# Kernel optimization log

Measured on AMD Instinct MI355X. Metric: run time of the kernel, lower is better.

## Reference

```python
import jax, jax.numpy as jnp
import numpy as np
from math import factorial

D = 2          # qudit dimension
L = 13         # number of qudits: state dim = D**L = 8192
J, K = 0, 1    # levels coupled by the gate
CUTOFF = 10    # Taylor truncation order
INDEX = set(range(13))


def _series(z, parity):
    # sum_{i=1..CUTOFF, i%2==parity} z**i / i!   (truncated exp split into even/odd parts)
    s = jnp.zeros((), dtype=jnp.complex64)
    for i in range(1, CUTOFF + 1):
        if i % 2 == parity:
            s = s + z ** i / factorial(i)
    return s


def _gate(theta):
    # single-qudit RX gate matrix, truncated-Taylor version matching the torch code
    z = (-0.5j) * theta.astype(jnp.complex64)
    odd = _series(z, 1)   # ~ -i sin(theta/2)
    even = _series(z, 0)  # ~ cos(theta/2) - 1
    M = jnp.eye(D, dtype=jnp.complex64)
    M = M.at[J, K].add(odd)
    M = M.at[K, J].add(odd)
    M = M.at[J, J].add(even)
    M = M.at[K, K].add(even)
    return M


def setup_inputs() -> dict:
    key = jax.random.key(0)
    k1, k2, k3 = jax.random.split(key, 3)
    dim = D ** L
    return {
        "x_real": jax.random.normal(k1, (dim, 64), dtype=jnp.float32),
        "x_imag": jax.random.normal(k2, (dim, 64), dtype=jnp.float32),
        "angle": jax.random.normal(k3, (L,), dtype=jnp.float32),
    }


def reference(x_real, x_imag, angle):
    x = x_real.astype(jnp.complex64) + 1j * x_imag.astype(jnp.complex64)
    eye = jnp.eye(D, dtype=jnp.complex64)
    U = jnp.eye(1, dtype=jnp.complex64)
    for i in range(L):  # fixed structural loop over qudits (13 iterations)
        M = _gate(angle[i]) if i in INDEX else eye
        U = jnp.kron(U, M)
    out = U @ x  # [D^L, B] complex64
    return jnp.stack([out.real, out.imag])  # [2, D^L, B] float32
```

## Files before the change

kernel.cpp:

```cpp
#include <hip/hip_runtime.h>

#define PLANE (8192 * 64)

typedef float f4 __attribute__((ext_vector_type(4)));
typedef float f2 __attribute__((ext_vector_type(2)));

__device__ __forceinline__ void gate_coeffs(float theta, float& a, float& s) {
    float t = 0.5f * theta;
    float u = t * t;
    s = t * (1.f + u * (-1.f/6.f + u * (1.f/120.f + u * (-1.f/5040.f + u * (1.f/362880.f)))));
    a = 1.f + u * (-0.5f + u * (1.f/24.f + u * (-1.f/720.f + u * (1.f/40320.f + u * (-1.f/3628800.f)))));
}

__device__ __forceinline__ void bf(f4& v0, f4& v1, float a, float s) {
    f4 n0, n1;
    n0.x = a * v0.x + s * v1.y;  n0.y = a * v0.y - s * v1.x;
    n0.z = a * v0.z + s * v1.w;  n0.w = a * v0.w - s * v1.z;
    n1.x = a * v1.x + s * v0.y;  n1.y = a * v1.y - s * v0.x;
    n1.z = a * v1.z + s * v0.w;  n1.w = a * v1.w - s * v0.z;
    v0 = n0; v1 = n1;
}

__global__ __launch_bounds__(256) void rx_low(const float* __restrict__ xr,
                                              const float* __restrict__ xi,
                                              const float* __restrict__ angle,
                                              f4* __restrict__ ws4) {
    __shared__ f4 l4[64 * 16];
    const int t = threadIdx.x, bid = blockIdx.x;
    const int g = bid >> 1, half = bid & 1;
    const int cp = t & 15, rq = t >> 4;

    const f2* xr2 = (const f2*)xr;
    const f2* xi2 = (const f2*)xi;

    {
        float a0, s0, a1, s1;
        gate_coeffs(angle[12], a0, s0);
        gate_coeffs(angle[11], a1, s1);
        f4 v[4];
        #pragma unroll
        for (int k = 0; k < 4; ++k) {
            int gi = (g * 64 + 4 * rq + k) * 32 + half * 16 + cp;
            f2 re = __builtin_nontemporal_load(xr2 + gi);
            f2 im = __builtin_nontemporal_load(xi2 + gi);
            v[k] = (f4){re.x, im.x, re.y, im.y};
        }
        bf(v[0], v[1], a0, s0); bf(v[2], v[3], a0, s0);
        bf(v[0], v[2], a1, s1); bf(v[1], v[3], a1, s1);
        #pragma unroll
        for (int k = 0; k < 4; ++k) l4[(4 * rq + k) * 16 + cp] = v[k];
    }
    __syncthreads();

    {
        float a2, s2, a3, s3;
        gate_coeffs(angle[10], a2, s2);
        gate_coeffs(angle[9],  a3, s3);
        int base = ((rq >> 2) << 4) | (rq & 3);
        f4 w0 = l4[(base     ) * 16 + cp], w1 = l4[(base +  4) * 16 + cp];
        f4 w2 = l4[(base +  8) * 16 + cp], w3 = l4[(base + 12) * 16 + cp];
        bf(w0, w1, a2, s2); bf(w2, w3, a2, s2);
        bf(w0, w2, a3, s3); bf(w1, w3, a3, s3);
        l4[(base     ) * 16 + cp] = w0; l4[(base +  4) * 16 + cp] = w1;
        l4[(base +  8) * 16 + cp] = w2; l4[(base + 12) * 16 + cp] = w3;
    }
    __syncthreads();

    {
        float a4, s4, a5, s5;
        gate_coeffs(angle[8], a4, s4);
        gate_coeffs(angle[7], a5, s5);
        f4 w0 = l4[(rq     ) * 16 + cp], w1 = l4[(rq + 16) * 16 + cp];
        f4 w2 = l4[(rq + 32) * 16 + cp], w3 = l4[(rq + 48) * 16 + cp];
        bf(w0, w1, a4, s4); bf(w2, w3, a4, s4);
        bf(w0, w2, a5, s5); bf(w1, w3, a5, s5);
        const int cp32 = half * 16 + cp, q = cp32 >> 3, cb = cp32 & 7;
        const int e = g * 8 + cb;
        ws4[(size_t)((rq     ) * 4 + q) * 1024 + e] = w0;
        ws4[(size_t)((rq + 16) * 4 + q) * 1024 + e] = w1;
        ws4[(size_t)((rq + 32) * 4 + q) * 1024 + e] = w2;
        ws4[(size_t)((rq + 48) * 4 + q) * 1024 + e] = w3;
    }
}

__global__ __launch_bounds__(256) void rx_high(const float* __restrict__ angle,
                                               const f4* __restrict__ ws4,
                                               float* __restrict__ out) {
    __shared__ f4 l4[128 * 8];
    const int t = threadIdx.x, bid = blockIdx.x;
    const int m = bid >> 2, q = bid & 3;
    const int cp = t & 7, hq = t >> 3;

    {
        float a5, s5, a6, s6;
        gate_coeffs(angle[1], a5, s5);
        gate_coeffs(angle[0], a6, s6);
        const f4* src = ws4 + (size_t)(m * 4 + q) * 1024;
        f4 v0 = src[(hq     ) * 8 + cp], v1 = src[(hq + 32) * 8 + cp];
        f4 v2 = src[(hq + 64) * 8 + cp], v3 = src[(hq + 96) * 8 + cp];
        bf(v0, v1, a5, s5); bf(v2, v3, a5, s5);
        bf(v0, v2, a6, s6); bf(v1, v3, a6, s6);
        l4[(hq     ) * 8 + cp] = v0; l4[(hq + 32) * 8 + cp] = v1;
        l4[(hq + 64) * 8 + cp] = v2; l4[(hq + 96) * 8 + cp] = v3;
    }
    __syncthreads();

    {
        float a3, s3, a4, s4;
        gate_coeffs(angle[3], a3, s3);
        gate_coeffs(angle[2], a4, s4);
        int base = ((hq >> 3) << 5) | (hq & 7);
        f4 w0 = l4[(base     ) * 8 + cp], w1 = l4[(base +  8) * 8 + cp];
        f4 w2 = l4[(base + 16) * 8 + cp], w3 = l4[(base + 24) * 8 + cp];
        bf(w0, w1, a3, s3); bf(w2, w3, a3, s3);
        bf(w0, w2, a4, s4); bf(w1, w3, a4, s4);
        l4[(base     ) * 8 + cp] = w0; l4[(base +  8) * 8 + cp] = w1;
        l4[(base + 16) * 8 + cp] = w2; l4[(base + 24) * 8 + cp] = w3;
    }
    __syncthreads();

    {
        float a1, s1, a2, s2;
        gate_coeffs(angle[5], a1, s1);
        gate_coeffs(angle[4], a2, s2);
        int b = ((hq >> 1) << 3) | (hq & 1);
        f4 w0 = l4[(b    ) * 8 + cp], w1 = l4[(b + 2) * 8 + cp];
        f4 w2 = l4[(b + 4) * 8 + cp], w3 = l4[(b + 6) * 8 + cp];
        bf(w0, w1, a1, s1); bf(w2, w3, a1, s1);
        bf(w0, w2, a2, s2); bf(w1, w3, a2, s2);
        l4[(b    ) * 8 + cp] = w0; l4[(b + 2) * 8 + cp] = w1;
        l4[(b + 4) * 8 + cp] = w2; l4[(b + 6) * 8 + cp] = w3;
    }
    __syncthreads();

    {
        float a0, s0;
        gate_coeffs(angle[6], a0, s0);
        const int hp = t >> 2, cq = t & 3;
        f4 u0 = l4[(2 * hp) * 8 + 2 * cq],     u1 = l4[(2 * hp) * 8 + 2 * cq + 1];
        f4 v0 = l4[(2 * hp + 1) * 8 + 2 * cq], v1 = l4[(2 * hp + 1) * 8 + 2 * cq + 1];
        bf(u0, v0, a0, s0);
        bf(u1, v1, a0, s0);
        f4* outre4 = (f4*)out;
        f4* outim4 = (f4*)(out + PLANE);
        int o = ((2 * hp) * 64 + m) * 16 + q * 4 + cq;
        __builtin_nontemporal_store((f4){u0.x, u0.z, u1.x, u1.z}, outre4 + o);
        __builtin_nontemporal_store((f4){u0.y, u0.w, u1.y, u1.w}, outim4 + o);
        __builtin_nontemporal_store((f4){v0.x, v0.z, v1.x, v1.z}, outre4 + o + 1024);
        __builtin_nontemporal_store((f4){v0.y, v0.w, v1.y, v1.w}, outim4 + o + 1024);
    }
}

extern "C" void kernel_launch(void* const* d_in, const int* in_sizes, int n_in,
                              void* d_out, int out_size, void* d_ws, size_t ws_size,
                              hipStream_t stream) {
    const float* xr    = (const float*)d_in[0];
    const float* xi    = (const float*)d_in[1];
    const float* angle = (const float*)d_in[2];
    float* out = (float*)d_out;
    f4*    ws4 = (f4*)d_ws;

    rx_low <<<256, 256, 0, stream>>>(xr, xi, angle, ws4);
    rx_high<<<256, 256, 0, stream>>>(angle, ws4, out);
}
```

Measured before the change: 14.04 us.

## Fuse two passes into one persistent kernel partitioned per XCD with atomic work queues

Replaces the two-kernel low/high split with a single kernel. Each block reads its XCC_ID and takes work items from per-XCD atomic counters. The intermediate stays in an XCD-local workspace slice written and read with sc0 (L2-scoped) accesses, and a per-XCD spin barrier separates the two phases. The aim is to save the second kernel launch and keep the intermediate in the XCD's L2, and the LDS is swizzled to cut bank conflicts. In exchange it adds a memset launch, atomic and barrier overhead, and it relies on an equal number of blocks landing on every XCD, with a bounded spin-wait as the only fallback.

```diff
diff --git a/kernel.cpp b/kernel.cpp
--- a/kernel.cpp
+++ b/kernel.cpp
@@ -21,133 +21,195 @@
     v0 = n0; v1 = n1;
 }
 
-__global__ __launch_bounds__(256) void rx_low(const float* __restrict__ xr,
+__device__ __forceinline__ int slotB(int h, int c) { return h * 8 + (c ^ (h & 7)); }
+
+__global__ __launch_bounds__(256) void rx_xcd(const float* __restrict__ xr,
                                               const float* __restrict__ xi,
                                               const float* __restrict__ angle,
-                                              f4* __restrict__ ws4) {
-    __shared__ f4 l4[64 * 16];
-    const int t = threadIdx.x, bid = blockIdx.x;
-    const int g = bid >> 1, half = bid & 1;
-    const int cp = t & 15, rq = t >> 4;
+                                              f4* __restrict__ ws4,
+                                              unsigned int* __restrict__ cnt,
+                                              float* __restrict__ out) {
+    __shared__ f4 l4[1024];
+    __shared__ int sh_idx;
+    const int t = threadIdx.x;
+
+    unsigned int xid;
+    asm volatile("s_getreg_b32 %0, hwreg(HW_REG_XCC_ID)" : "=s"(xid));
+    const int x = (int)(xid & 7u);
+
+    f4* wsx = ws4 + (size_t)x * 32768;
+    unsigned int* aq = cnt + x * 16;
+    unsigned int* ad = cnt + 128 + x * 16;
+    unsigned int* bq = cnt + 256 + x * 16;
 
     const f2* xr2 = (const f2*)xr;
     const f2* xi2 = (const f2*)xi;
 
-    {
-        float a0, s0, a1, s1;
-        gate_coeffs(angle[12], a0, s0);
-        gate_coeffs(angle[11], a1, s1);
-        f4 v[4];
-        #pragma unroll
-        for (int k = 0; k < 4; ++k) {
-            int gi = (g * 64 + 4 * rq + k) * 32 + half * 16 + cp;
-            f2 re = __builtin_nontemporal_load(xr2 + gi);
-            f2 im = __builtin_nontemporal_load(xi2 + gi);
-            v[k] = (f4){re.x, im.x, re.y, im.y};
-        }
-        bf(v[0], v[1], a0, s0); bf(v[2], v[3], a0, s0);
-        bf(v[0], v[2], a1, s1); bf(v[1], v[3], a1, s1);
-        #pragma unroll
-        for (int k = 0; k < 4; ++k) l4[(4 * rq + k) * 16 + cp] = v[k];
+    for (;;) {
+        __syncthreads();
+        if (t == 0)
+            sh_idx = (int)__hip_atomic_fetch_add(aq, 1u, __ATOMIC_RELAXED,
+                                                 __HIP_MEMORY_SCOPE_AGENT);
+        __syncthreads();
+        const int j = sh_idx;
+        if (j >= 32) break;
+
+        const int col = t & 15, rq = t >> 4;
+        const int grp = col >> 2, cq = col & 3;
+        const int h = 4 * j + grp;
+
+        {
+            float a0, s0, a1, s1;
+            gate_coeffs(angle[12], a0, s0);
+            gate_coeffs(angle[11], a1, s1);
+            int gb = (h * 64 + 4 * rq) * 32 + x * 4 + cq;
+            f2 re, im; f4 v0, v1, v2, v3;
+            re = __builtin_nontemporal_load(xr2 + gb);
+            im = __builtin_nontemporal_load(xi2 + gb);      v0 = (f4){re.x, im.x, re.y, im.y};
+            re = __builtin_nontemporal_load(xr2 + gb + 32);
+            im = __builtin_nontemporal_load(xi2 + gb + 32); v1 = (f4){re.x, im.x, re.y, im.y};
+            re = __builtin_nontemporal_load(xr2 + gb + 64);
+            im = __builtin_nontemporal_load(xi2 + gb + 64); v2 = (f4){re.x, im.x, re.y, im.y};
+            re = __builtin_nontemporal_load(xr2 + gb + 96);
+            im = __builtin_nontemporal_load(xi2 + gb + 96); v3 = (f4){re.x, im.x, re.y, im.y};
+            bf(v0, v1, a0, s0); bf(v2, v3, a0, s0);
+            bf(v0, v2, a1, s1); bf(v1, v3, a1, s1);
+            l4[(4 * rq + 0) * 16 + col] = v0;
+            l4[(4 * rq + 1) * 16 + col] = v1;
+            l4[(4 * rq + 2) * 16 + col] = v2;
+            l4[(4 * rq + 3) * 16 + col] = v3;
+        }
+        __syncthreads();
+
+        {
+            float a2, s2, a3, s3;
+            gate_coeffs(angle[10], a2, s2);
+            gate_coeffs(angle[9],  a3, s3);
+            int base = ((rq >> 2) << 4) | (rq & 3);
+            f4 w0 = l4[(base     ) * 16 + col], w1 = l4[(base +  4) * 16 + col];
+            f4 w2 = l4[(base +  8) * 16 + col], w3 = l4[(base + 12) * 16 + col];
+            bf(w0, w1, a2, s2); bf(w2, w3, a2, s2);
+            bf(w0, w2, a3, s3); bf(w1, w3, a3, s3);
+            l4[(base     ) * 16 + col] = w0; l4[(base +  4) * 16 + col] = w1;
+            l4[(base +  8) * 16 + col] = w2; l4[(base + 12) * 16 + col] = w3;
+        }
+        __syncthreads();
+
+        {
+            float a4, s4, a5, s5;
+            gate_coeffs(angle[8], a4, s4);
+            gate_coeffs(angle[7], a5, s5);
+            f4 w0 = l4[(rq     ) * 16 + col], w1 = l4[(rq + 16) * 16 + col];
+            f4 w2 = l4[(rq + 32) * 16 + col], w3 = l4[(rq + 48) * 16 + col];
+            bf(w0, w1, a4, s4); bf(w2, w3, a4, s4);
+            bf(w0, w2, a5, s5); bf(w1, w3, a5, s5);
+            const f4* p0 = wsx + ((size_t)((rq     ) * 4 + cq) * 128 + h);
+            const f4* p1 = wsx + ((size_t)((rq + 16) * 4 + cq) * 128 + h);
+            const f4* p2 = wsx + ((size_t)((rq + 32) * 4 + cq) * 128 + h);
+            const f4* p3 = wsx + ((size_t)((rq + 48) * 4 + cq) * 128 + h);
+            asm volatile("global_store_dwordx4 %0, %4, off sc0\n\t"
+                         "global_store_dwordx4 %1, %5, off sc0\n\t"
+                         "global_store_dwordx4 %2, %6, off sc0\n\t"
+                         "global_store_dwordx4 %3, %7, off sc0"
+                         :: "v"(p0), "v"(p1), "v"(p2), "v"(p3),
+                            "v"(w0), "v"(w1), "v"(w2), "v"(w3) : "memory");
+        }
+        asm volatile("s_waitcnt vmcnt(0)" ::: "memory");
+        __syncthreads();
+        if (t == 0)
+            __hip_atomic_fetch_add(ad, 1u, __ATOMIC_RELAXED, __HIP_MEMORY_SCOPE_AGENT);
+    }
+
+    if (t == 0) {
+        int guard = 0;
+        while (__hip_atomic_load(ad, __ATOMIC_RELAXED, __HIP_MEMORY_SCOPE_AGENT) < 32u
+               && ++guard < 2000000)
+            __builtin_amdgcn_s_sleep(8);
     }
     __syncthreads();
 
-    {
-        float a2, s2, a3, s3;
-        gate_coeffs(angle[10], a2, s2);
-        gate_coeffs(angle[9],  a3, s3);
-        int base = ((rq >> 2) << 4) | (rq & 3);
-        f4 w0 = l4[(base     ) * 16 + cp], w1 = l4[(base +  4) * 16 + cp];
-        f4 w2 = l4[(base +  8) * 16 + cp], w3 = l4[(base + 12) * 16 + cp];
-        bf(w0, w1, a2, s2); bf(w2, w3, a2, s2);
-        bf(w0, w2, a3, s3); bf(w1, w3, a3, s3);
-        l4[(base     ) * 16 + cp] = w0; l4[(base +  4) * 16 + cp] = w1;
-        l4[(base +  8) * 16 + cp] = w2; l4[(base + 12) * 16 + cp] = w3;
-    }
-    __syncthreads();
-
-    {
-        float a4, s4, a5, s5;
-        gate_coeffs(angle[8], a4, s4);
-        gate_coeffs(angle[7], a5, s5);
-        f4 w0 = l4[(rq     ) * 16 + cp], w1 = l4[(rq + 16) * 16 + cp];
-        f4 w2 = l4[(rq + 32) * 16 + cp], w3 = l4[(rq + 48) * 16 + cp];
-        bf(w0, w1, a4, s4); bf(w2, w3, a4, s4);
-        bf(w0, w2, a5, s5); bf(w1, w3, a5, s5);
-        const int cp32 = half * 16 + cp, q = cp32 >> 3, cb = cp32 & 7;
-        const int e = g * 8 + cb;
-        ws4[(size_t)((rq     ) * 4 + q) * 1024 + e] = w0;
-        ws4[(size_t)((rq + 16) * 4 + q) * 1024 + e] = w1;
-        ws4[(size_t)((rq + 32) * 4 + q) * 1024 + e] = w2;
-        ws4[(size_t)((rq + 48) * 4 + q) * 1024 + e] = w3;
-    }
-}
-
-__global__ __launch_bounds__(256) void rx_high(const float* __restrict__ angle,
-                                               const f4* __restrict__ ws4,
-                                               float* __restrict__ out) {
-    __shared__ f4 l4[128 * 8];
-    const int t = threadIdx.x, bid = blockIdx.x;
-    const int m = bid >> 2, q = bid & 3;
-    const int cp = t & 7, hq = t >> 3;
-
-    {
-        float a5, s5, a6, s6;
-        gate_coeffs(angle[1], a5, s5);
-        gate_coeffs(angle[0], a6, s6);
-        const f4* src = ws4 + (size_t)(m * 4 + q) * 1024;
-        f4 v0 = src[(hq     ) * 8 + cp], v1 = src[(hq + 32) * 8 + cp];
-        f4 v2 = src[(hq + 64) * 8 + cp], v3 = src[(hq + 96) * 8 + cp];
-        bf(v0, v1, a5, s5); bf(v2, v3, a5, s5);
-        bf(v0, v2, a6, s6); bf(v1, v3, a6, s6);
-        l4[(hq     ) * 8 + cp] = v0; l4[(hq + 32) * 8 + cp] = v1;
-        l4[(hq + 64) * 8 + cp] = v2; l4[(hq + 96) * 8 + cp] = v3;
-    }
-    __syncthreads();
-
-    {
-        float a3, s3, a4, s4;
-        gate_coeffs(angle[3], a3, s3);
-        gate_coeffs(angle[2], a4, s4);
-        int base = ((hq >> 3) << 5) | (hq & 7);
-        f4 w0 = l4[(base     ) * 8 + cp], w1 = l4[(base +  8) * 8 + cp];
-        f4 w2 = l4[(base + 16) * 8 + cp], w3 = l4[(base + 24) * 8 + cp];
-        bf(w0, w1, a3, s3); bf(w2, w3, a3, s3);
-        bf(w0, w2, a4, s4); bf(w1, w3, a4, s4);
-        l4[(base     ) * 8 + cp] = w0; l4[(base +  8) * 8 + cp] = w1;
-        l4[(base + 16) * 8 + cp] = w2; l4[(base + 24) * 8 + cp] = w3;
-    }
-    __syncthreads();
-
-    {
-        float a1, s1, a2, s2;
-        gate_coeffs(angle[5], a1, s1);
-        gate_coeffs(angle[4], a2, s2);
-        int b = ((hq >> 1) << 3) | (hq & 1);
-        f4 w0 = l4[(b    ) * 8 + cp], w1 = l4[(b + 2) * 8 + cp];
-        f4 w2 = l4[(b + 4) * 8 + cp], w3 = l4[(b + 6) * 8 + cp];
-        bf(w0, w1, a1, s1); bf(w2, w3, a1, s1);
-        bf(w0, w2, a2, s2); bf(w1, w3, a2, s2);
-        l4[(b    ) * 8 + cp] = w0; l4[(b + 2) * 8 + cp] = w1;
-        l4[(b + 4) * 8 + cp] = w2; l4[(b + 6) * 8 + cp] = w3;
-    }
-    __syncthreads();
-
-    {
-        float a0, s0;
-        gate_coeffs(angle[6], a0, s0);
-        const int hp = t >> 2, cq = t & 3;
-        f4 u0 = l4[(2 * hp) * 8 + 2 * cq],     u1 = l4[(2 * hp) * 8 + 2 * cq + 1];
-        f4 v0 = l4[(2 * hp + 1) * 8 + 2 * cq], v1 = l4[(2 * hp + 1) * 8 + 2 * cq + 1];
-        bf(u0, v0, a0, s0);
-        bf(u1, v1, a0, s0);
-        f4* outre4 = (f4*)out;
-        f4* outim4 = (f4*)(out + PLANE);
-        int o = ((2 * hp) * 64 + m) * 16 + q * 4 + cq;
-        __builtin_nontemporal_store((f4){u0.x, u0.z, u1.x, u1.z}, outre4 + o);
-        __builtin_nontemporal_store((f4){u0.y, u0.w, u1.y, u1.w}, outim4 + o);
-        __builtin_nontemporal_store((f4){v0.x, v0.z, v1.x, v1.z}, outre4 + o + 1024);
-        __builtin_nontemporal_store((f4){v0.y, v0.w, v1.y, v1.w}, outim4 + o + 1024);
+    for (;;) {
+        __syncthreads();
+        if (t == 0)
+            sh_idx = (int)__hip_atomic_fetch_add(bq, 1u, __ATOMIC_RELAXED,
+                                                 __HIP_MEMORY_SCOPE_AGENT);
+        __syncthreads();
+        const int j = sh_idx;
+        if (j >= 32) break;
+
+        {
+            float a5, s5, a6, s6;
+            gate_coeffs(angle[1], a5, s5);
+            gate_coeffs(angle[0], a6, s6);
+            const int hL = t & 31, cB = t >> 5;
+            const f4* src = wsx + (size_t)j * 1024 + cB * 128 + hL;
+            f4 v0, v1, v2, v3;
+            asm volatile("global_load_dwordx4 %0, %4, off sc0\n\t"
+                         "global_load_dwordx4 %1, %5, off sc0\n\t"
+                         "global_load_dwordx4 %2, %6, off sc0\n\t"
+                         "global_load_dwordx4 %3, %7, off sc0\n\t"
+                         "s_waitcnt vmcnt(0)"
+                         : "=&v"(v0), "=&v"(v1), "=&v"(v2), "=&v"(v3)
+                         : "v"(src), "v"(src + 32), "v"(src + 64), "v"(src + 96)
+                         : "memory");
+            bf(v0, v1, a5, s5); bf(v2, v3, a5, s5);
+            bf(v0, v2, a6, s6); bf(v1, v3, a6, s6);
+            l4[slotB(hL,      cB)] = v0;
+            l4[slotB(hL + 32, cB)] = v1;
+            l4[slotB(hL + 64, cB)] = v2;
+            l4[slotB(hL + 96, cB)] = v3;
+        }
+        __syncthreads();
+
+        {
+            float a3, s3, a4, s4;
+            gate_coeffs(angle[3], a3, s3);
+            gate_coeffs(angle[2], a4, s4);
+            const int cB = t & 7, hq = t >> 3;
+            int base = ((hq >> 3) << 5) | (hq & 7);
+            f4 w0 = l4[slotB(base,      cB)], w1 = l4[slotB(base +  8, cB)];
+            f4 w2 = l4[slotB(base + 16, cB)], w3 = l4[slotB(base + 24, cB)];
+            bf(w0, w1, a3, s3); bf(w2, w3, a3, s3);
+            bf(w0, w2, a4, s4); bf(w1, w3, a4, s4);
+            l4[slotB(base,      cB)] = w0; l4[slotB(base +  8, cB)] = w1;
+            l4[slotB(base + 16, cB)] = w2; l4[slotB(base + 24, cB)] = w3;
+        }
+        __syncthreads();
+
+        {
+            float a1, s1, a2, s2;
+            gate_coeffs(angle[5], a1, s1);
+            gate_coeffs(angle[4], a2, s2);
+            const int cB = t & 7, hq = t >> 3;
+            int b = ((hq >> 1) << 3) | (hq & 1);
+            f4 w0 = l4[slotB(b,     cB)], w1 = l4[slotB(b + 2, cB)];
+            f4 w2 = l4[slotB(b + 4, cB)], w3 = l4[slotB(b + 6, cB)];
+            bf(w0, w1, a1, s1); bf(w2, w3, a1, s1);
+            bf(w0, w2, a2, s2); bf(w1, w3, a2, s2);
+            l4[slotB(b,     cB)] = w0; l4[slotB(b + 2, cB)] = w1;
+            l4[slotB(b + 4, cB)] = w2; l4[slotB(b + 6, cB)] = w3;
+        }
+        __syncthreads();
+
+        {
+            float a0, s0;
+            gate_coeffs(angle[6], a0, s0);
+            const int hd = t >> 2, u = t & 3;
+            const int mo = u >> 1, cqh = u & 1;
+            const int c0 = mo * 4 + 2 * cqh, c1 = c0 + 1;
+            f4 u0 = l4[slotB(2 * hd,     c0)], u1 = l4[slotB(2 * hd,     c1)];
+            f4 v0 = l4[slotB(2 * hd + 1, c0)], v1 = l4[slotB(2 * hd + 1, c1)];
+            bf(u0, v0, a0, s0);
+            bf(u1, v1, a0, s0);
+            f4* outre4 = (f4*)out;
+            f4* outim4 = (f4*)(out + PLANE);
+            const int m = 2 * j + mo;
+            int o = ((2 * hd) * 64 + m) * 16 + x * 2 + cqh;
+            __builtin_nontemporal_store((f4){u0.x, u0.z, u1.x, u1.z}, outre4 + o);
+            __builtin_nontemporal_store((f4){u0.y, u0.w, u1.y, u1.w}, outim4 + o);
+            __builtin_nontemporal_store((f4){v0.x, v0.z, v1.x, v1.z}, outre4 + o + 1024);
+            __builtin_nontemporal_store((f4){v0.y, v0.w, v1.y, v1.w}, outim4 + o + 1024);
+        }
     }
 }
 
@@ -159,7 +221,8 @@
     const float* angle = (const float*)d_in[2];
     float* out = (float*)d_out;
     f4*    ws4 = (f4*)d_ws;
-
-    rx_low <<<256, 256, 0, stream>>>(xr, xi, angle, ws4);
-    rx_high<<<256, 256, 0, stream>>>(angle, ws4, out);
-}
+    unsigned int* cnt = (unsigned int*)((char*)d_ws + (4u << 20));
+
+    hipMemsetAsync(cnt, 0, 1536, stream);
+    rx_xcd<<<256, 256, 0, stream>>>(xr, xi, angle, ws4, cnt, out);
+}
```

Result: slower. 21.49 us (+53.1%).
